# Optimization experiments

Hardware: AMD Instinct MI355X
Metric: run time of the kernel (lower is better)

## Reference

```python
import jax, jax.numpy as jnp
import numpy as np

B = 65536
QUERY_DIM = 1024
CROSS_DIM = 1024
HEADS = 16
DIM_HEAD = 64
INNER = HEADS * DIM_HEAD  # 1024
SCALE = DIM_HEAD ** -0.5


def setup_inputs() -> dict:
    key = jax.random.key(0)
    ks = jax.random.split(key, 7)
    s_in = 1.0 / np.sqrt(QUERY_DIM)
    s_c = 1.0 / np.sqrt(CROSS_DIM)
    s_o = 1.0 / np.sqrt(INNER)
    return {
        "latent": jax.random.normal(ks[0], (B, QUERY_DIM), jnp.float32),
        "cond_latent": jax.random.normal(ks[1], (B, CROSS_DIM), jnp.float32),
        "Wq": jax.random.normal(ks[2], (INNER, QUERY_DIM), jnp.float32) * s_in,
        "Wk": jax.random.normal(ks[3], (INNER, CROSS_DIM), jnp.float32) * s_c,
        "Wv": jax.random.normal(ks[4], (INNER, CROSS_DIM), jnp.float32) * s_c,
        "Wout": jax.random.normal(ks[5], (QUERY_DIM, INNER), jnp.float32) * s_o,
        "bout": jax.random.normal(ks[6], (QUERY_DIM,), jnp.float32) * s_o,
    }


def reference(latent, cond_latent, Wq, Wk, Wv, Wout, bout):
    # projections: [B, inner] -> [B, heads, dim_head]
    Q = (latent @ Wq.T).reshape(B, HEADS, DIM_HEAD)
    K = (cond_latent @ Wk.T).reshape(B, HEADS, DIM_HEAD)
    V = (cond_latent @ Wv.T).reshape(B, HEADS, DIM_HEAD)
    # attention across the heads axis: scores [B, heads, heads]
    scores = jnp.einsum("bhd,bgd->bhg", Q, K) * SCALE
    probs = jax.nn.softmax(scores, axis=-1)
    feats = jnp.einsum("bhg,bgd->bhd", probs, V).reshape(B, INNER)
    return feats @ Wout.T + bout
```

## Files before the change

### kernel.cpp

```cpp
#include <hip/hip_runtime.h>
#include <hip/hip_bf16.h>

#define NB    65536
#define KDIM  1024
#define NDIM  1024

#define BK 32
#define NT (KDIM / BK)

typedef float f32x4  __attribute__((ext_vector_type(4)));
typedef short short8 __attribute__((ext_vector_type(8)));
typedef unsigned short ushort8v __attribute__((ext_vector_type(8)));

static __device__ __forceinline__ unsigned short f2bf(float f) {
    union { float f; unsigned u; } v; v.f = f;
    unsigned r = v.u + 0x7FFFu + ((v.u >> 16) & 1u);
    return (unsigned short)(r >> 16);
}
static __device__ __forceinline__ float bf2f(unsigned short h) {
    union { unsigned u; float f; } v; v.u = ((unsigned)h) << 16;
    return v.f;
}

static __device__ __forceinline__ void gload16(const unsigned short* g, unsigned short* l) {
    __builtin_amdgcn_global_load_lds(
        (const __attribute__((address_space(1))) unsigned int*)g,
        (__attribute__((address_space(3))) unsigned int*)l, 16, 0, 0);
}


__global__ __launch_bounds__(256) void pack_all_k(
    const float* __restrict__ latent, const float* __restrict__ cond,
    const float* __restrict__ Wq, const float* __restrict__ Wk,
    const float* __restrict__ Wv, const float* __restrict__ Wout,
    unsigned short* __restrict__ Lp, unsigned short* __restrict__ Cp,
    unsigned short* __restrict__ wqp, unsigned short* __restrict__ wkvp,
    unsigned short* __restrict__ wop)
{
    const int b = blockIdx.x;
    const float* src; unsigned short* dst; int rb;
    if (b < 4096)      { src = latent; dst = Lp;              rb = b; }
    else if (b < 8192) { src = cond;   dst = Cp;              rb = b - 4096; }
    else if (b < 8256) { src = Wq;     dst = wqp;             rb = b - 8192; }
    else if (b < 8320) { src = Wk;     dst = wkvp;            rb = b - 8256; }
    else if (b < 8384) { src = Wv;     dst = wkvp + 1048576;  rb = b - 8320; }
    else               { src = Wout;   dst = wop;             rb = b - 8384; }

    const int tid = threadIdx.x;
    const int r   = rb * 16 + (tid >> 4);
    const int cb  = (tid & 15) * 64;
    const int p   = r >> 8;
    const int f   = (r >> 4) & 15;
    const int rl  = r & 15;
    const float* s = src + (size_t)r * 1024 + cb;
#pragma unroll
    for (int g = 0; g < 8; ++g) {
        float4 va = *reinterpret_cast<const float4*>(s + g * 8);
        float4 vb = *reinterpret_cast<const float4*>(s + g * 8 + 4);
        ushort8v o;
        o[0] = f2bf(va.x); o[1] = f2bf(va.y); o[2] = f2bf(va.z); o[3] = f2bf(va.w);
        o[4] = f2bf(vb.x); o[5] = f2bf(vb.y); o[6] = f2bf(vb.z); o[7] = f2bf(vb.w);
        const int c0 = cb + g * 8;
        const int t  = c0 >> 5;
        const int kc = (c0 & 31) >> 3;
        *reinterpret_cast<ushort8v*>(
            &dst[((size_t)(p * 32 + t) * 16 + f) * 512 + kc * 128 + rl * 8]) = o;
    }
}

typedef unsigned short ldsT[4][2][16][512];

static __device__ __forceinline__ void gemm_core(
    const unsigned short* __restrict__ Ap, const unsigned short* __restrict__ Wp,
    int pA, int pB, int lane, int wid, int wm, int wn,
    ldsT& lds, f32x4 (&acc)[8][4])
{
#define STAGE1_(TAU, SLOT, AB) do {                                             \
        int _tc = (TAU) < NT ? (TAU) : NT - 1;                                  \
        const unsigned short* _b = (AB) ? Wp : Ap;                              \
        int _pp = (AB) ? pB : pA;                                               \
        _Pragma("unroll")                                                       \
        for (int _j = 0; _j < 2; ++_j) {                                        \
            int _f = wid * 2 + _j;                                              \
            gload16(_b + ((size_t)(_pp * 32 + _tc) * 16 + _f) * 512 + lane * 8, \
                    &lds[SLOT][AB][_f][0]);                                     \
        }                                                                       \
    } while (0)

#define LDA_(S, MI) \
    (*reinterpret_cast<const short8*>(&lds[S][0][wm * 8 + (MI)][lane * 8]))
#define LDB_(S, NI) \
    (*reinterpret_cast<const short8*>(&lds[S][1][wn * 4 + (NI)][lane * 8]))

    STAGE1_(0, 0, 0); STAGE1_(0, 0, 1);
    STAGE1_(1, 1, 0); STAGE1_(1, 1, 1);
    STAGE1_(2, 2, 0); STAGE1_(2, 2, 1);
    asm volatile("s_waitcnt vmcnt(8)" ::: "memory");
    __builtin_amdgcn_s_barrier();

#pragma unroll 1
    for (int tt = 0; tt < NT; ++tt) {
        const int slot = tt & 3;
        short8 af0[4], af1[4], bq[4];

#pragma unroll
        for (int mi = 0; mi < 4; ++mi) af0[mi] = LDA_(slot, mi);
#pragma unroll
        for (int ni = 0; ni < 4; ++ni) bq[ni] = LDB_(slot, ni);
        STAGE1_(tt + 3, (tt + 3) & 3, 0);
        __builtin_amdgcn_s_barrier();
        asm volatile("s_waitcnt lgkmcnt(0)" ::: "memory");
        __builtin_amdgcn_s_setprio(1);
#pragma unroll
        for (int mi = 0; mi < 4; ++mi)
#pragma unroll
            for (int ni = 0; ni < 4; ++ni)
                acc[mi][ni] = __builtin_amdgcn_mfma_f32_16x16x32_bf16(
                    af0[mi], bq[ni], acc[mi][ni], 0, 0, 0);
        __builtin_amdgcn_s_setprio(0);
        __builtin_amdgcn_s_barrier();

#pragma unroll
        for (int mi = 0; mi < 4; ++mi) af1[mi] = LDA_(slot, 4 + mi);
        STAGE1_(tt + 3, (tt + 3) & 3, 1);
        asm volatile("s_waitcnt vmcnt(8)" ::: "memory");
        __builtin_amdgcn_s_barrier();
        asm volatile("s_waitcnt lgkmcnt(0)" ::: "memory");
        __builtin_amdgcn_s_setprio(1);
#pragma unroll
        for (int mi = 0; mi < 4; ++mi)
#pragma unroll
            for (int ni = 0; ni < 4; ++ni)
                acc[4 + mi][ni] = __builtin_amdgcn_mfma_f32_16x16x32_bf16(
                    af1[mi], bq[ni], acc[4 + mi][ni], 0, 0, 0);
        __builtin_amdgcn_s_setprio(0);
        __builtin_amdgcn_s_barrier();
    }
    asm volatile("s_waitcnt vmcnt(0)" ::: "memory");
    __builtin_amdgcn_s_barrier();
#undef STAGE1_
#undef LDA_
#undef LDB_
}

__global__ __launch_bounds__(512, 2) void gemm_qkv(
    const unsigned short* __restrict__ Lp, const unsigned short* __restrict__ Cp,
    const unsigned short* __restrict__ wqp, const unsigned short* __restrict__ wkvp,
    unsigned short* __restrict__ Qb, unsigned short* __restrict__ KVb)
{
    __shared__ alignas(16) ldsT lds;

    const int t    = threadIdx.x;
    const int lane = t & 63;
    const int wid  = t >> 6;
    const int wm   = wid >> 2;
    const int wn   = wid & 3;

    const int nwg  = gridDim.x;
    const int cpx  = nwg >> 3;
    const int orig = blockIdx.x;
    const int wgid = (orig & 7) * cpx + (orig >> 3);

    const unsigned short* Ap; const unsigned short* Wp;
    unsigned short* Cb; int NN, bn0, bm0;
    if (wgid < 1024) {
        Ap = Lp; Wp = wqp; Cb = Qb; NN = 1024;
        bn0 = (wgid & 3) * 256; bm0 = (wgid >> 2) * 256;
    } else {
        int w2 = wgid - 1024;
        Ap = Cp; Wp = wkvp; Cb = KVb; NN = 2048;
        bn0 = (w2 & 7) * 256; bm0 = (w2 >> 3) * 256;
    }
    const int pA = bm0 >> 8, pB = bn0 >> 8;

    f32x4 acc[8][4];
#pragma unroll
    for (int mi = 0; mi < 8; ++mi)
#pragma unroll
        for (int ni = 0; ni < 4; ++ni)
            acc[mi][ni] = (f32x4){0.f, 0.f, 0.f, 0.f};

    gemm_core(Ap, Wp, pA, pB, lane, wid, wm, wn, lds, acc);

    const int crow = (lane >> 4) * 4;
    const int ccol = lane & 15;
    unsigned short* bb = &lds[0][0][0][0];
#pragma unroll
    for (int p = 0; p < 2; ++p) {
        if (wm == p) {
#pragma unroll
            for (int ml = 0; ml < 8; ++ml)
#pragma unroll
                for (int ni = 0; ni < 4; ++ni)
#pragma unroll
                    for (int r = 0; r < 4; ++r)
                        bb[(ml * 16 + crow + r) * 264 + wn * 64 + ni * 16 + ccol]
                            = f2bf(acc[ml][ni][r]);
        }
        __syncthreads();
#pragma unroll
        for (int it = 0; it < 8; ++it) {
            int lrow = wid * 16 + it * 2 + (lane >> 5);
            int lcol = (lane & 31) * 8;
            ushort8v v = *reinterpret_cast<const ushort8v*>(&bb[lrow * 264 + lcol]);
            *reinterpret_cast<ushort8v*>(
                &Cb[(size_t)(bm0 + p * 128 + lrow) * NN + bn0 + lcol]) = v;
        }
        __syncthreads();
    }
}

__global__ __launch_bounds__(512, 2) void gemm_out(
    const unsigned short* __restrict__ Fp, const unsigned short* __restrict__ wop,
    const float* __restrict__ bias, float* __restrict__ Cf)
{
    constexpr int NN = 1024;
    __shared__ alignas(16) ldsT lds;

    const int t    = threadIdx.x;
    const int lane = t & 63;
    const int wid  = t >> 6;
    const int wm   = wid >> 2;
    const int wn   = wid & 3;

    const int nwg  = gridDim.x;
    const int cpx  = nwg >> 3;
    const int orig = blockIdx.x;
    const int wgid = (orig & 7) * cpx + (orig >> 3);
    const int bn0  = (wgid & 3) * 256;
    const int bm0  = (wgid >> 2) * 256;
    const int pA = bm0 >> 8, pB = bn0 >> 8;

    f32x4 acc[8][4];
#pragma unroll
    for (int mi = 0; mi < 8; ++mi)
#pragma unroll
        for (int ni = 0; ni < 4; ++ni)
            acc[mi][ni] = (f32x4){0.f, 0.f, 0.f, 0.f};

    gemm_core(Fp, wop, pA, pB, lane, wid, wm, wn, lds, acc);

    const int crow = (lane >> 4) * 4;
    const int ccol = lane & 15;
    float* bbf = reinterpret_cast<float*>(&lds[0][0][0][0]);
    float bv[4];
#pragma unroll
    for (int ni = 0; ni < 4; ++ni)
        bv[ni] = bias[bn0 + wn * 64 + ni * 16 + ccol];
#pragma unroll
    for (int p = 0; p < 4; ++p) {
        if (wm == (p >> 1)) {
#pragma unroll
            for (int ml = 0; ml < 4; ++ml)
#pragma unroll
                for (int ni = 0; ni < 4; ++ni)
#pragma unroll
                    for (int r = 0; r < 4; ++r)
                        bbf[(ml * 16 + crow + r) * 268 + wn * 64 + ni * 16 + ccol]
                            = acc[(p & 1) * 4 + ml][ni][r] + bv[ni];
        }
        __syncthreads();
#pragma unroll
        for (int it = 0; it < 8; ++it) {
            int lrow = wid * 8 + it;
            f32x4 v = *reinterpret_cast<const f32x4*>(&bbf[lrow * 268 + lane * 4]);
            *reinterpret_cast<f32x4*>(
                &Cf[(size_t)(bm0 + p * 64 + lrow) * NN + bn0 + lane * 4]) = v;
        }
        __syncthreads();
    }
}

__global__ __launch_bounds__(1024) void attn_k(
    const unsigned short* __restrict__ Qb, const unsigned short* __restrict__ KVb,
    unsigned short* __restrict__ Fp)
{
    __shared__ alignas(16) unsigned short KL[16][1024];
    __shared__ alignas(16) unsigned short VL[16][1024];
    const int t = threadIdx.x;
    const int lane = t & 63;
    const int wid = t >> 6;
    const size_t row = (size_t)blockIdx.x * 16 + wid;
    const size_t base = row * 1024;
    const size_t bkv  = row * 2048;
    const int off = lane * 16;

    ushort8v q0 = *reinterpret_cast<const ushort8v*>(&Qb[base + off]);
    ushort8v q1 = *reinterpret_cast<const ushort8v*>(&Qb[base + off + 8]);
    float qf[16];
#pragma unroll
    for (int j = 0; j < 8; ++j) { qf[j] = bf2f(q0[j]); qf[8 + j] = bf2f(q1[j]); }

    *reinterpret_cast<ushort8v*>(&KL[wid][off])     = *reinterpret_cast<const ushort8v*>(&KVb[bkv + off]);
    *reinterpret_cast<ushort8v*>(&KL[wid][off + 8]) = *reinterpret_cast<const ushort8v*>(&KVb[bkv + off + 8]);
    *reinterpret_cast<ushort8v*>(&VL[wid][off])     = *reinterpret_cast<const ushort8v*>(&KVb[bkv + 1024 + off]);
    *reinterpret_cast<ushort8v*>(&VL[wid][off + 8]) = *reinterpret_cast<const ushort8v*>(&KVb[bkv + 1024 + off + 8]);
    __syncthreads();

    const int sub = lane & 3;
    float s[16];
#pragma unroll
    for (int g = 0; g < 16; ++g) {
        const ushort8v k0 = *reinterpret_cast<const ushort8v*>(&KL[wid][g * 64 + sub * 16]);
        const ushort8v k1 = *reinterpret_cast<const ushort8v*>(&KL[wid][g * 64 + sub * 16 + 8]);
        float acc = 0.f;
#pragma unroll
        for (int j = 0; j < 8; ++j)
            acc += qf[j] * bf2f(k0[j]) + qf[8 + j] * bf2f(k1[j]);
        s[g] = acc;
    }
#pragma unroll
    for (int m = 1; m <= 2; m <<= 1)
#pragma unroll
        for (int g = 0; g < 16; ++g)
            s[g] += __shfl_xor(s[g], m, 64);

    float mx = s[0];
#pragma unroll
    for (int g = 1; g < 16; ++g) mx = fmaxf(mx, s[g]);
    float p[16], denom = 0.f;
#pragma unroll
    for (int g = 0; g < 16; ++g) {
        p[g] = __expf((s[g] - mx) * 0.125f);
        denom += p[g];
    }
    float inv = 1.f / denom;

    float f[16];
#pragma unroll
    for (int j = 0; j < 16; ++j) f[j] = 0.f;
#pragma unroll
    for (int g = 0; g < 16; ++g) {
        float pg = p[g] * inv;
        const ushort8v v0 = *reinterpret_cast<const ushort8v*>(&VL[wid][g * 64 + sub * 16]);
        const ushort8v v1 = *reinterpret_cast<const ushort8v*>(&VL[wid][g * 64 + sub * 16 + 8]);
#pragma unroll
        for (int j = 0; j < 8; ++j) {
            f[j]     += pg * bf2f(v0[j]);
            f[8 + j] += pg * bf2f(v1[j]);
        }
    }
    ushort8v o0, o1;
#pragma unroll
    for (int j = 0; j < 8; ++j) { o0[j] = f2bf(f[j]); o1[j] = f2bf(f[8 + j]); }
    *reinterpret_cast<ushort8v*>(&KL[wid][off])     = o0;
    *reinterpret_cast<ushort8v*>(&KL[wid][off + 8]) = o1;
    __syncthreads();

    const int r0 = blockIdx.x * 16;
    const int pp = r0 >> 8;
    const int ff = (r0 >> 4) & 15;
    const int tt = t >> 5;
    const int kc = (t >> 3) & 3;
    const int rp = t & 7;
    unsigned short* db = &Fp[((size_t)(pp * 32 + tt) * 16 + ff) * 512 + kc * 128 + rp * 16];
    *reinterpret_cast<ushort8v*>(db)     = *reinterpret_cast<const ushort8v*>(&KL[rp * 2][tt * 32 + kc * 8]);
    *reinterpret_cast<ushort8v*>(db + 8) = *reinterpret_cast<const ushort8v*>(&KL[rp * 2 + 1][tt * 32 + kc * 8]);
}

extern "C" void kernel_launch(void* const* d_in, const int* in_sizes, int n_in,
                              void* d_out, int out_size, void* d_ws, size_t ws_size,
                              hipStream_t stream)
{
    (void)in_sizes; (void)n_in; (void)out_size; (void)ws_size;
    const float* latent = (const float*)d_in[0];
    const float* cond   = (const float*)d_in[1];
    const float* Wq     = (const float*)d_in[2];
    const float* Wk     = (const float*)d_in[3];
    const float* Wv     = (const float*)d_in[4];
    const float* Wout   = (const float*)d_in[5];
    const float* bout   = (const float*)d_in[6];
    float* out = (float*)d_out;

    char* ws = (char*)d_ws;
    const size_t MB = 1ull << 20;
    unsigned short* wqp  = (unsigned short*)(ws + 0 * MB);
    unsigned short* wkvp = (unsigned short*)(ws + 2 * MB);
    unsigned short* wop  = (unsigned short*)(ws + 6 * MB);
    unsigned short* Qb   = (unsigned short*)(ws + 8 * MB);
    unsigned short* KVb  = (unsigned short*)(ws + 136 * MB);
    unsigned short* Lp   = (unsigned short*)(ws + 392 * MB);
    unsigned short* Cp   = (unsigned short*)(ws + 520 * MB);
    unsigned short* Fp   = Lp;

    pack_all_k<<<8448, 256, 0, stream>>>(latent, cond, Wq, Wk, Wv, Wout,
                                         Lp, Cp, wqp, wkvp, wop);

    gemm_qkv<<<3072, 512, 0, stream>>>(Lp, Cp, wqp, wkvp, Qb, KVb);

    attn_k<<<NB / 16, 1024, 0, stream>>>(Qb, KVb, Fp);

    gemm_out<<<1024, 512, 0, stream>>>(Fp, wop, bout, out);
}
```

Measured before the change: 967.7 us.

## Load A fragments directly to registers and double-buffer only B in LDS

Reworks the GEMM core so each wave loads its A-operand fragments straight from global memory into registers, since each wave's A rows are private. Only the shared B (weight) tile is staged through a two-slot LDS ring. This shrinks LDS use and removes A traffic through LDS. The trade-off is a shallower prefetch, waiting on vmcnt(0) each half-step, plus more register pressure from two full A fragment sets, so global latency may be less hidden.

```diff
diff --git a/kernel.cpp b/kernel.cpp
--- a/kernel.cpp
+++ b/kernel.cpp
@@ -68,79 +68,77 @@
     }
 }
 
-typedef unsigned short ldsT[4][2][16][512];
-
-static __device__ __forceinline__ void gemm_core(
+typedef unsigned short ringT[2][16][512];
+
+static __device__ __forceinline__ void gemm_core2(
     const unsigned short* __restrict__ Ap, const unsigned short* __restrict__ Wp,
     int pA, int pB, int lane, int wid, int wm, int wn,
-    ldsT& lds, f32x4 (&acc)[8][4])
-{
-#define STAGE1_(TAU, SLOT, AB) do {                                             \
-        int _tc = (TAU) < NT ? (TAU) : NT - 1;                                  \
-        const unsigned short* _b = (AB) ? Wp : Ap;                              \
-        int _pp = (AB) ? pB : pA;                                               \
+    unsigned short* smem, f32x4 (&acc)[8][4])
+{
+    ringT& ring = *reinterpret_cast<ringT*>(smem);
+    const unsigned short* baseA =
+        Ap + ((size_t)(pA * 32) * 16 + wm * 8) * 512 + lane * 8;
+
+#define STAGEB_(TAU, SLOT) do {                                                 \
         _Pragma("unroll")                                                       \
         for (int _j = 0; _j < 2; ++_j) {                                        \
             int _f = wid * 2 + _j;                                              \
-            gload16(_b + ((size_t)(_pp * 32 + _tc) * 16 + _f) * 512 + lane * 8, \
-                    &lds[SLOT][AB][_f][0]);                                     \
+            gload16(Wp + ((size_t)(pB * 32 + (TAU)) * 16 + _f) * 512 + lane * 8,\
+                    &ring[SLOT][_f][0]);                                        \
         }                                                                       \
     } while (0)
 
-#define LDA_(S, MI) \
-    (*reinterpret_cast<const short8*>(&lds[S][0][wm * 8 + (MI)][lane * 8]))
-#define LDB_(S, NI) \
-    (*reinterpret_cast<const short8*>(&lds[S][1][wn * 4 + (NI)][lane * 8]))
-
-    STAGE1_(0, 0, 0); STAGE1_(0, 0, 1);
-    STAGE1_(1, 1, 0); STAGE1_(1, 1, 1);
-    STAGE1_(2, 2, 0); STAGE1_(2, 2, 1);
-    asm volatile("s_waitcnt vmcnt(8)" ::: "memory");
-    __builtin_amdgcn_s_barrier();
-
-#pragma unroll 1
-    for (int tt = 0; tt < NT; ++tt) {
-        const int slot = tt & 3;
-        short8 af0[4], af1[4], bq[4];
-
-#pragma unroll
-        for (int mi = 0; mi < 4; ++mi) af0[mi] = LDA_(slot, mi);
-#pragma unroll
-        for (int ni = 0; ni < 4; ++ni) bq[ni] = LDB_(slot, ni);
-        STAGE1_(tt + 3, (tt + 3) & 3, 0);
-        __builtin_amdgcn_s_barrier();
-        asm volatile("s_waitcnt lgkmcnt(0)" ::: "memory");
-        __builtin_amdgcn_s_setprio(1);
-#pragma unroll
-        for (int mi = 0; mi < 4; ++mi)
-#pragma unroll
-            for (int ni = 0; ni < 4; ++ni)
-                acc[mi][ni] = __builtin_amdgcn_mfma_f32_16x16x32_bf16(
-                    af0[mi], bq[ni], acc[mi][ni], 0, 0, 0);
-        __builtin_amdgcn_s_setprio(0);
-        __builtin_amdgcn_s_barrier();
-
-#pragma unroll
-        for (int mi = 0; mi < 4; ++mi) af1[mi] = LDA_(slot, 4 + mi);
-        STAGE1_(tt + 3, (tt + 3) & 3, 1);
-        asm volatile("s_waitcnt vmcnt(8)" ::: "memory");
-        __builtin_amdgcn_s_barrier();
-        asm volatile("s_waitcnt lgkmcnt(0)" ::: "memory");
-        __builtin_amdgcn_s_setprio(1);
-#pragma unroll
-        for (int mi = 0; mi < 4; ++mi)
-#pragma unroll
-            for (int ni = 0; ni < 4; ++ni)
-                acc[4 + mi][ni] = __builtin_amdgcn_mfma_f32_16x16x32_bf16(
-                    af1[mi], bq[ni], acc[4 + mi][ni], 0, 0, 0);
-        __builtin_amdgcn_s_setprio(0);
-        __builtin_amdgcn_s_barrier();
-    }
+#define LOADA_(T, AA) do {                                                      \
+        _Pragma("unroll")                                                       \
+        for (int _mi = 0; _mi < 8; ++_mi)                                       \
+            AA[_mi] = *reinterpret_cast<const short8*>(                         \
+                baseA + (size_t)(T) * 8192 + _mi * 512);                        \
+    } while (0)
+
+#define READB_(SLOT, BQ) do {                                                   \
+        _Pragma("unroll")                                                       \
+        for (int _ni = 0; _ni < 4; ++_ni)                                       \
+            BQ[_ni] = *reinterpret_cast<const short8*>(                         \
+                &ring[SLOT][wn * 4 + _ni][lane * 8]);                           \
+    } while (0)
+
+#define MFMA_(AA, BQ) do {                                                      \
+        __builtin_amdgcn_s_setprio(1);                                          \
+        _Pragma("unroll")                                                       \
+        for (int _mi = 0; _mi < 8; ++_mi)                                       \
+            _Pragma("unroll")                                                   \
+            for (int _ni = 0; _ni < 4; ++_ni)                                   \
+                acc[_mi][_ni] = __builtin_amdgcn_mfma_f32_16x16x32_bf16(        \
+                    AA[_mi], BQ[_ni], acc[_mi][_ni], 0, 0, 0);                  \
+        __builtin_amdgcn_s_setprio(0);                                          \
+    } while (0)
+
+    short8 aA[8], aB[8], bq[4];
+
+    LOADA_(0, aA);
+    STAGEB_(0, 0);
     asm volatile("s_waitcnt vmcnt(0)" ::: "memory");
     __builtin_amdgcn_s_barrier();
-#undef STAGE1_
-#undef LDA_
-#undef LDB_
+
+#pragma unroll 1
+    for (int tt = 0; tt < NT; tt += 2) {
+        LOADA_(tt + 1, aB);
+        STAGEB_(tt + 1, 1);
+        READB_(0, bq);
+        MFMA_(aA, bq);
+        asm volatile("s_waitcnt vmcnt(0)" ::: "memory");
+        __builtin_amdgcn_s_barrier();
+
+        if (tt + 2 < NT) { LOADA_(tt + 2, aA); STAGEB_(tt + 2, 0); }
+        READB_(1, bq);
+        MFMA_(aB, bq);
+        asm volatile("s_waitcnt vmcnt(0)" ::: "memory");
+        __builtin_amdgcn_s_barrier();
+    }
+#undef STAGEB_
+#undef LOADA_
+#undef READB_
+#undef MFMA_
 }
 
 __global__ __launch_bounds__(512, 2) void gemm_qkv(
@@ -148,7 +146,7 @@
     const unsigned short* __restrict__ wqp, const unsigned short* __restrict__ wkvp,
     unsigned short* __restrict__ Qb, unsigned short* __restrict__ KVb)
 {
-    __shared__ alignas(16) ldsT lds;
+    __shared__ alignas(16) unsigned short smem[33792];
 
     const int t    = threadIdx.x;
     const int lane = t & 63;
@@ -180,11 +178,11 @@
         for (int ni = 0; ni < 4; ++ni)
             acc[mi][ni] = (f32x4){0.f, 0.f, 0.f, 0.f};
 
-    gemm_core(Ap, Wp, pA, pB, lane, wid, wm, wn, lds, acc);
+    gemm_core2(Ap, Wp, pA, pB, lane, wid, wm, wn, smem, acc);
 
     const int crow = (lane >> 4) * 4;
     const int ccol = lane & 15;
-    unsigned short* bb = &lds[0][0][0][0];
+    unsigned short* bb = smem;
 #pragma unroll
     for (int p = 0; p < 2; ++p) {
         if (wm == p) {
@@ -215,7 +213,7 @@
     const float* __restrict__ bias, float* __restrict__ Cf)
 {
     constexpr int NN = 1024;
-    __shared__ alignas(16) ldsT lds;
+    __shared__ alignas(16) unsigned short smem[34304];
 
     const int t    = threadIdx.x;
     const int lane = t & 63;
@@ -238,11 +236,11 @@
         for (int ni = 0; ni < 4; ++ni)
             acc[mi][ni] = (f32x4){0.f, 0.f, 0.f, 0.f};
 
-    gemm_core(Fp, wop, pA, pB, lane, wid, wm, wn, lds, acc);
+    gemm_core2(Fp, wop, pA, pB, lane, wid, wm, wn, smem, acc);
 
     const int crow = (lane >> 4) * 4;
     const int ccol = lane & 15;
-    float* bbf = reinterpret_cast<float*>(&lds[0][0][0][0]);
+    float* bbf = reinterpret_cast<float*>(smem);
     float bv[4];
 #pragma unroll
     for (int ni = 0; ni < 4; ++ni)
```

Measured after the change: 1.211 ms. +25.1%, slower.
